# Kernel optimization log

Hardware: AMD Instinct MI355X
Metric: run time of the kernel (lower is better)

## Reference

```python
import jax, jax.numpy as jnp
import numpy as np

LEAK = 0.2
TEMP = 0.1          # CausalMask temperature
SPARSITY_W = 0.1
MI_W = 0.01
DAG_W = 1.0

def _leaky(x):
    return jax.nn.leaky_relu(x, LEAK)

def setup_inputs() -> dict:
    key = jax.random.key(0)
    B, F, S, H = 4096, 512, 32, 512
    H2, CH = H // 2, 64
    P = S * (S - 1) // 2  # 496 MI estimators
    ks = jax.random.split(key, 32)
    def w(k, shape, fan_in):
        return jax.random.normal(k, shape, jnp.float32) / np.sqrt(fan_in)
    return {
        'features': jax.random.normal(ks[0], (B, F), jnp.float32),
        'eps':      jax.random.normal(ks[1], (B, S), jnp.float32),
        'enc_w1': w(ks[2], (F, H), F),   'enc_b1': w(ks[3], (H,), H),
        'enc_w2': w(ks[4], (H, 2 * S), H), 'enc_b2': w(ks[5], (2 * S,), H) * 0.1,
        'log_weight': jax.random.normal(ks[6], (S, S), jnp.float32) * 0.5,
        'mech_w1': w(ks[7], (S, S, H2), S), 'mech_b1': w(ks[8], (S, H2), H2),
        'mech_w2': w(ks[9], (S, H2), H2),   'mech_b2': w(ks[10], (S,), H2),
        'dec_w1': w(ks[11], (S, H), S),  'dec_b1': w(ks[12], (H,), H),
        'dec_w2': w(ks[13], (H, F), H),  'dec_b2': w(ks[14], (F,), H),
        'mi_w1': w(ks[15], (P, 2, CH), 2),  'mi_b1': w(ks[16], (P, CH), CH),
        'mi_w2': w(ks[17], (P, CH, CH), CH), 'mi_b2': w(ks[18], (P, CH), CH),
        'mi_w3': w(ks[19], (P, CH), CH),     'mi_b3': w(ks[20], (P,), CH),
    }

def _forward(features, eps, enc_w1, enc_b1, enc_w2, enc_b2, log_weight,
             mech_w1, mech_b1, mech_w2, mech_b2, dec_w1, dec_b1, dec_w2, dec_b2,
             mi_w1, mi_b1, mi_w2, mi_b2, mi_w3, mi_b3):
    S = log_weight.shape[0]
    # ---- encode ----
    h = _leaky(features @ enc_w1 + enc_b1)
    params = h @ enc_w2 + enc_b2
    mean, log_std = jnp.split(params, 2, axis=-1)
    std = jnp.exp(log_std)
    z = mean + std * eps                                   # [B,S]
    # ---- soft causal adjacency (training mode) ----
    eye = jnp.eye(S, dtype=features.dtype)
    upper = jnp.triu(jnp.ones((S, S), features.dtype), k=1)
    lw = log_weight * upper - 10.0 * eye
    A = jax.nn.sigmoid(lw / TEMP)                          # [S,S]
    # ---- apply_causal_structure: stoch_dim tiny MLPs, vectorized ----
    # z_parents[b,i,s] = z[b,s] * A[s,i]
    zp = z[:, None, :] * A.T[None, :, :]                   # [B,S,S]
    h1 = _leaky(jnp.einsum('bis,ish->bih', zp, mech_w1) + mech_b1)  # [B,S,H2]
    z_causal = jnp.einsum('bih,ih->bi', h1, mech_w2) + mech_b2      # [B,S]
    # ---- decode ----
    recon = _leaky(z_causal @ dec_w1 + dec_b1) @ dec_w2 + dec_b2    # [B,F]
    # ---- losses ----
    recon_loss = jnp.mean((recon - features) ** 2)
    kl_loss = 0.5 * jnp.sum(mean ** 2 + std ** 2 - 2.0 * log_std - 1.0, axis=-1).mean()
    Asig = jax.nn.sigmoid(log_weight)
    sparsity_loss = jnp.sum(jnp.abs(Asig))
    # MI: one tiny MLP per (i<j) pair, row-major order == torch loop order
    iu, ju = jnp.triu_indices(S, k=1)
    pair = jnp.stack([z[:, iu], z[:, ju]], axis=-1)        # [B,P,2]
    m1 = _leaky(jnp.einsum('bpi,pih->bph', pair, mi_w1) + mi_b1)
    m2 = _leaky(jnp.einsum('bph,phk->bpk', m1, mi_w2) + mi_b2)
    mi_est = (jnp.einsum('bph,ph->bp', m2, mi_w3) + mi_b3).mean(0)  # [P]
    mi_loss = jnp.sum(jax.nn.sigmoid(log_weight[iu, ju]) * mi_est)
    # DAG: truncated matrix-exponential trace penalty
    A2 = Asig * Asig
    expm = eye
    mp = eye
    fact = 1.0
    for i in range(1, 10):
        fact *= i
        mp = mp @ A2
        expm = expm + mp / fact
    dag_loss = (jnp.trace(expm) - S) ** 2
    total_loss = recon_loss + kl_loss + SPARSITY_W * sparsity_loss + MI_W * mi_loss + DAG_W * dag_loss
    return z_causal, mean, std, recon, total_loss, recon_loss, kl_loss, sparsity_loss, mi_loss, dag_loss

def reference(features, eps, enc_w1, enc_b1, enc_w2, enc_b2, log_weight,
              mech_w1, mech_b1, mech_w2, mech_b2, dec_w1, dec_b1, dec_w2, dec_b2,
              mi_w1, mi_b1, mi_w2, mi_b2, mi_w3, mi_b3):
    return _forward(features, eps, enc_w1, enc_b1, enc_w2, enc_b2, log_weight,
                    mech_w1, mech_b1, mech_w2, mech_b2, dec_w1, dec_b1, dec_w2, dec_b2,
                    mi_w1, mi_b1, mi_w2, mi_b2, mi_w3, mi_b3)
```

## Files before the change

kernel.cpp:

```cpp
#include <hip/hip_runtime.h>
#include <hip/hip_bf16.h>

typedef float f32x4 __attribute__((ext_vector_type(4)));
typedef float f32x2 __attribute__((ext_vector_type(2)));
typedef short s16x8 __attribute__((ext_vector_type(8)));

__device__ __forceinline__ float leaky2(float x){ return fmaf(0.4f, fabsf(x), 0.6f * x); }

__device__ __forceinline__ short f2bf(float f){
    return __builtin_bit_cast(short, __float2bfloat16(f));
}

__global__ __launch_bounds__(256) void k_cvt(
    const float* __restrict__ feat, const float* __restrict__ ew1,
    const float* __restrict__ ew2, const float* __restrict__ dw2,
    const float* __restrict__ mw1, const float* __restrict__ mw2,
    const float* __restrict__ dw1,
    short* __restrict__ featbf, short* __restrict__ w1p,
    short* __restrict__ ew2p, short* __restrict__ dw2p,
    short* __restrict__ mw1p, short* __restrict__ mw2p,
    short* __restrict__ dw1p,
    const float* __restrict__ lw, float* __restrict__ A,
    float* __restrict__ acc)
{
    if (blockIdx.x >= 2048){
        __shared__ float A2s[1024], mp[1024], red[256];
        const int t = threadIdx.x;
        acc[t] = 0.f;
        acc[t + 256] = 0.f;
        float part = 0.f;
        #pragma unroll
        for (int q = 0; q < 4; ++q){
            int e = t * 4 + q;
            int r = e >> 5, c = e & 31;
            float v = lw[e];
            float sig = 1.f / (1.f + expf(-v));
            float l2 = (r < c) ? v * 10.f : ((r == c) ? -100.f : 0.f);
            A[e] = 1.f / (1.f + expf(-l2));
            part += sig;
            float a2 = sig * sig;
            A2s[e] = a2; mp[e] = a2;
        }
        red[t] = part; __syncthreads();
        for (int s = 128; s > 0; s >>= 1){ if (t < s) red[t] += red[t + s]; __syncthreads(); }
        if (t == 0) acc[2] = red[0];

        const float invf[10] = {0.f, 1.f, 0.5f, 1.6666667e-1f, 4.1666667e-2f,
                                8.3333333e-3f, 1.3888889e-3f, 1.9841270e-4f,
                                2.4801587e-5f, 2.7557319e-6f};
        float tr = 0.f;
        const int r = t >> 3, c0 = (t & 7) * 4;
        for (int n = 1; n <= 9; ++n){
            __syncthreads();
            if (t == 0){
                float s = 0.f;
                for (int k2 = 0; k2 < 32; ++k2) s += mp[k2 * 33];
                tr += s * invf[n];
            }
            if (n == 9) break;
            float av[4] = {0.f, 0.f, 0.f, 0.f};
            for (int k2 = 0; k2 < 32; ++k2){
                float m = mp[r * 32 + k2];
                #pragma unroll
                for (int q = 0; q < 4; ++q) av[q] = fmaf(m, A2s[k2 * 32 + c0 + q], av[q]);
            }
            __syncthreads();
            #pragma unroll
            for (int q = 0; q < 4; ++q) mp[r * 32 + c0 + q] = av[q];
        }
        if (t == 0) acc[3] = tr * tr;
        return;
    }
    for (int idx = blockIdx.x * 256 + threadIdx.x; idx < 620544; idx += 2048 * 256){
        int d = idx * 8;
        if (d < 2097152){
            f32x4 a0 = *(const f32x4*)&feat[d];
            f32x4 a1 = *(const f32x4*)&feat[d + 4];
            s16x8 v;
            #pragma unroll
            for (int e = 0; e < 4; ++e){ v[e] = f2bf(a0[e]); v[e + 4] = f2bf(a1[e]); }
            *(s16x8*)&featbf[d] = v;
            continue;
        }
        int s = d - 2097152;
        if (s < 262144){
            int t2 = s >> 9, lane = (s & 511) >> 3;
            int kb = (t2 & 15) * 32 + (lane >> 4) * 8;
            int n  = (t2 >> 4) * 16 + (lane & 15);
            s16x8 v;
            #pragma unroll
            for (int e = 0; e < 8; ++e) v[e] = f2bf(ew1[(kb + e) * 512 + n]);
            *(s16x8*)&w1p[s] = v;
            continue;
        }
        s -= 262144;
        if (s < 32768){
            int t2 = s >> 9, lane = (s & 511) >> 3;
            int kb = (t2 & 15) * 32 + (lane >> 4) * 8;
            int n  = (t2 >> 4) * 16 + (lane & 15);
            s16x8 v;
            #pragma unroll
            for (int e = 0; e < 8; ++e) v[e] = f2bf(ew2[(kb + e) * 64 + n]);
            *(s16x8*)&ew2p[s] = v;
            continue;
        }
        s -= 32768;
        if (s < 262144){
            int t2 = s >> 9, lane = (s & 511) >> 3;
            int kb = (t2 & 15) * 32 + (lane >> 4) * 8;
            int n  = (t2 >> 4) * 16 + (lane & 15);
            s16x8 v;
            #pragma unroll
            for (int e = 0; e < 8; ++e) v[e] = f2bf(dw2[(kb + e) * 512 + n]);
            *(s16x8*)&dw2p[s] = v;
            continue;
        }
        s -= 262144;
        if (s < 262144){
            int i = s >> 13, r2 = s & 8191;
            int nt = r2 >> 9, lane = (r2 & 511) >> 3;
            int kb = (lane >> 4) * 8;
            int n  = nt * 16 + (lane & 15);
            s16x8 v;
            #pragma unroll
            for (int e = 0; e < 8; ++e) v[e] = f2bf(mw1[i * 8192 + (kb + e) * 256 + n]);
            *(s16x8*)&mw1p[s] = v;
            continue;
        }
        s -= 262144;
        if (s < 2031616){
            int p = s >> 12, r2 = s & 4095;
            int tt = r2 >> 9, lane = (r2 & 511) >> 3;
            int nb = tt >> 1, ks = tt & 1;
            int kb = ks * 32 + (lane >> 4) * 8;
            int col = nb * 16 + (lane & 15);
            s16x8 v;
            #pragma unroll
            for (int e = 0; e < 8; ++e) v[e] = f2bf(mw2[(size_t)p * 4096 + (kb + e) * 64 + col]);
            *(s16x8*)&mw2p[s] = v;
            continue;
        }
        s -= 2031616;
        int nt = s >> 9, lane = (s & 511) >> 3;
        int kb = (lane >> 4) * 8;
        int n  = nt * 16 + (lane & 15);
        s16x8 v;
        #pragma unroll
        for (int e = 0; e < 8; ++e) v[e] = f2bf(dw1[(kb + e) * 512 + n]);
        *(s16x8*)&dw1p[s] = v;
    }
}

__global__ __launch_bounds__(512) void k_encf(
    const short* __restrict__ featbf, const short* __restrict__ w1p,
    const float* __restrict__ eb1, const short* __restrict__ ew2p,
    const float* __restrict__ eb2, const float* __restrict__ eps,
    float* __restrict__ omean, float* __restrict__ ostd,
    float* __restrict__ zt, float* __restrict__ accg)
{
    __shared__ short hlds[8192];
    __shared__ float P[16][65];
    __shared__ float zs[16][33];
    __shared__ float red[512];
    const int t = threadIdx.x, lane = t & 63, wv = t >> 6;
    const int ml = lane & 15, kg = lane >> 4;
    const int b0 = blockIdx.x * 16;

    f32x4 acc1[4] = {};
    for (int kt = 0; kt < 16; ++kt){
        s16x8 a = *(const s16x8*)&featbf[(size_t)(b0 + ml) * 512 + kt * 32 + kg * 8];
        #pragma unroll
        for (int nf = 0; nf < 4; ++nf){
            s16x8 b = *(const s16x8*)&w1p[((wv * 4 + nf) * 16 + kt) * 512 + lane * 8];
            acc1[nf] = __builtin_amdgcn_mfma_f32_16x16x32_bf16(a, b, acc1[nf], 0, 0, 0);
        }
    }
    #pragma unroll
    for (int nf = 0; nf < 4; ++nf){
        int col = wv * 64 + nf * 16 + ml;
        float bv = eb1[col];
        #pragma unroll
        for (int r = 0; r < 4; ++r){
            int row = kg * 4 + r;
            int byte = (row * 1024 + col * 2) ^ ((row & 7) << 4);
            hlds[byte >> 1] = f2bf(leaky2(acc1[nf][r] + bv));
        }
    }
    __syncthreads();

    if (wv < 4){
        f32x4 acc2 = {};
        for (int kt = 0; kt < 16; ++kt){
            int byte = (ml * 1024 + kt * 64 + kg * 16) ^ ((ml & 7) << 4);
            s16x8 a = *(const s16x8*)((const char*)hlds + byte);
            s16x8 b = *(const s16x8*)&ew2p[(wv * 16 + kt) * 512 + lane * 8];
            acc2 = __builtin_amdgcn_mfma_f32_16x16x32_bf16(a, b, acc2, 0, 0, 0);
        }
        int col = wv * 16 + ml;
        float bv = eb2[col];
        #pragma unroll
        for (int r = 0; r < 4; ++r)
            P[kg * 4 + r][col] = acc2[r] + bv;
    }
    __syncthreads();
    float klp = 0.f;
    {
        int row = t >> 5, n = t & 31;
        float mean = P[row][n], ls = P[row][n + 32];
        float sd = expf(ls);
        size_t o = (size_t)(b0 + row) * 32 + n;
        float z = fmaf(sd, eps[o], mean);
        omean[o] = mean; ostd[o] = sd;
        zs[row][n] = z;
        klp = mean * mean + sd * sd - 2.f * ls - 1.f;
    }
    __syncthreads();
    {
        int n = t >> 4, row = t & 15;
        zt[(size_t)n * 4096 + b0 + row] = zs[row][n];
    }
    red[t] = klp; __syncthreads();
    for (int s = 256; s > 0; s >>= 1){ if (t < s) red[t] += red[t + s]; __syncthreads(); }
    if (t == 0) atomicAdd(accg + 0, red[0]);
}

__global__ __launch_bounds__(256) void k_mimech(
    const float* __restrict__ zt,
    const float* __restrict__ w1g, const float* __restrict__ b1g,
    const short* __restrict__ w2p, const float* __restrict__ b2g,
    const float* __restrict__ w3g, float* __restrict__ macc,
    const float* __restrict__ A, const short* __restrict__ W1p,
    const float* __restrict__ mb1, const float* __restrict__ mw2,
    const float* __restrict__ mb2, float* __restrict__ out_zc)
{
    __shared__ float sA[32], sB1[256], sW2[256];
    const int t = threadIdx.x, lane = t & 63, wv = t >> 6;
    const int ml = lane & 15, kg = lane >> 4;
    if (blockIdx.x < 1984){
        const int p = blockIdx.x >> 2, bq = blockIdx.x & 3;
        int pi = 0, rem = p;
        while (rem >= 31 - pi){ rem -= 31 - pi; ++pi; }
        const int pj = pi + 1 + rem;

        const int zrow = wv * 16 + ml;
        const float* zi_b = zt + (size_t)pi * 4096 + bq * 1024 + zrow;
        const float* zj_b = zt + (size_t)pj * 4096 + bq * 1024 + zrow;

        f32x2 w10v[2][4], w11v[2][4], b1v[2][4];
        #pragma unroll
        for (int ks = 0; ks < 2; ++ks)
            #pragma unroll
            for (int q = 0; q < 4; ++q){
                int h = ks * 32 + kg * 8 + q * 2;
                w10v[ks][q] = *(const f32x2*)&w1g[p * 128 + h] * 0.6f;
                w11v[ks][q] = *(const f32x2*)&w1g[p * 128 + 64 + h] * 0.6f;
                b1v[ks][q]  = *(const f32x2*)&b1g[p * 64 + h] * 0.6f;
            }
        s16x8 bfr[4][2];
        f32x4 b2c[4];
        #pragma unroll
        for (int nb = 0; nb < 4; ++nb){
            float bv = b2g[p * 64 + nb * 16 + ml];
            b2c[nb][0] = bv; b2c[nb][1] = bv; b2c[nb][2] = bv; b2c[nb][3] = bv;
            #pragma unroll
            for (int ks = 0; ks < 2; ++ks)
                bfr[nb][ks] = *(const s16x8*)&w2p[(size_t)p * 4096 + (nb * 2 + ks) * 512 + lane * 8];
        }
        const f32x2 c23 = {0.66666669f, 0.66666669f};
        float slin[4] = {0.f, 0.f, 0.f, 0.f}, sabs[4] = {0.f, 0.f, 0.f, 0.f};
        #pragma unroll 1
        for (int tile = 0; tile < 16; ++tile){
            float zi_c = zi_b[tile * 64], zj_c = zj_b[tile * 64];
            f32x2 zi2 = {zi_c, zi_c}, zj2 = {zj_c, zj_c};
            s16x8 af0, af1;
            #pragma unroll
            for (int q = 0; q < 4; ++q){
                f32x2 m0 = __builtin_elementwise_fma(zi2, w10v[0][q],
                           __builtin_elementwise_fma(zj2, w11v[0][q], b1v[0][q]));
                m0 = __builtin_elementwise_fma(c23, __builtin_elementwise_abs(m0), m0);
                af0[q * 2] = f2bf(m0[0]); af0[q * 2 + 1] = f2bf(m0[1]);
                f32x2 m1 = __builtin_elementwise_fma(zi2, w10v[1][q],
                           __builtin_elementwise_fma(zj2, w11v[1][q], b1v[1][q]));
                m1 = __builtin_elementwise_fma(c23, __builtin_elementwise_abs(m1), m1);
                af1[q * 2] = f2bf(m1[0]); af1[q * 2 + 1] = f2bf(m1[1]);
            }
            #pragma unroll
            for (int nb = 0; nb < 4; ++nb){
                f32x4 d = __builtin_amdgcn_mfma_f32_16x16x32_bf16(af0, bfr[nb][0], b2c[nb], 0, 0, 0);
                d = __builtin_amdgcn_mfma_f32_16x16x32_bf16(af1, bfr[nb][1], d, 0, 0, 0);
                #pragma unroll
                for (int r2 = 0; r2 < 4; ++r2){
                    slin[nb] += d[r2];
                    sabs[nb] += fabsf(d[r2]);
                }
            }
        }
        float s = 0.f;
        #pragma unroll
        for (int nb = 0; nb < 4; ++nb){
            float w3 = w3g[p * 64 + nb * 16 + ml];
            s = fmaf(0.6f * w3, slin[nb], fmaf(0.4f * w3, sabs[nb], s));
        }
        #pragma unroll
        for (int off = 32; off; off >>= 1) s += __shfl_xor(s, off);
        if (lane == 0) atomicAdd(&macc[p], s);
    } else {
        const int bx = blockIdx.x - 1984;
        const int i = bx & 31;
        const int b0 = (bx >> 5) * 64 + wv * 16;
        if (t < 32) sA[t] = A[t * 32 + i];
        sB1[t] = mb1[i * 256 + t];
        sW2[t] = mw2[i * 256 + t];
        __syncthreads();
        float zv[8];
        #pragma unroll
        for (int q = 0; q < 8; ++q)
            zv[q] = zt[(size_t)(kg * 8 + q) * 4096 + b0 + ml];
        s16x8 af;
        #pragma unroll
        for (int q = 0; q < 8; ++q)
            af[q] = f2bf(zv[q] * sA[kg * 8 + q]);
        float s[4] = {0.f, 0.f, 0.f, 0.f};
        #pragma unroll
        for (int nt = 0; nt < 16; ++nt){
            s16x8 bf = *(const s16x8*)&W1p[i * 8192 + nt * 512 + lane * 8];
            int col = nt * 16 + ml;
            float b1e = sB1[col], w2v = sW2[col];
            f32x4 d;
            d[0] = b1e; d[1] = b1e; d[2] = b1e; d[3] = b1e;
            d = __builtin_amdgcn_mfma_f32_16x16x32_bf16(af, bf, d, 0, 0, 0);
            float w2a = 0.6f * w2v, w2b = 0.4f * w2v;
            #pragma unroll
            for (int r = 0; r < 4; ++r)
                s[r] = fmaf(w2a, d[r], fmaf(w2b, fabsf(d[r]), s[r]));
        }
        #pragma unroll
        for (int off = 1; off < 16; off <<= 1)
            #pragma unroll
            for (int r = 0; r < 4; ++r) s[r] += __shfl_xor(s[r], off);
        if (ml == 0){
            float bb = mb2[i];
            #pragma unroll
            for (int r = 0; r < 4; ++r){
                int b = b0 + kg * 4 + r;
                out_zc[(size_t)b * 32 + i] = s[r] + bb;
            }
        }
    }
}

__global__ __launch_bounds__(256) void k_decf(
    const float* __restrict__ zc, const short* __restrict__ dw1p,
    const float* __restrict__ db1, const short* __restrict__ dw2p,
    const float* __restrict__ db2, const float* __restrict__ feat,
    float* __restrict__ recon, float* __restrict__ accg)
{
    __shared__ short dlds[8192];
    __shared__ float red[256];
    const int t = threadIdx.x, lane = t & 63, wv = t >> 6;
    const int ml = lane & 15, kg = lane >> 4;
    const int b0 = blockIdx.x * 16;
    const int c0 = blockIdx.y * 128;

    s16x8 af;
    {
        int row = b0 + ml;
        f32x4 z0 = *(const f32x4*)&zc[(size_t)row * 32 + kg * 8];
        f32x4 z1 = *(const f32x4*)&zc[(size_t)row * 32 + kg * 8 + 4];
        #pragma unroll
        for (int e = 0; e < 4; ++e){
            af[e] = f2bf(z0[e]);
            af[e + 4] = f2bf(z1[e]);
        }
    }
    #pragma unroll
    for (int nf = 0; nf < 8; ++nf){
        int nt = wv * 8 + nf;
        s16x8 bf = *(const s16x8*)&dw1p[nt * 512 + lane * 8];
        int col = nt * 16 + ml;
        float b1e = db1[col];
        f32x4 c; c[0] = b1e; c[1] = b1e; c[2] = b1e; c[3] = b1e;
        f32x4 d = __builtin_amdgcn_mfma_f32_16x16x32_bf16(af, bf, c, 0, 0, 0);
        #pragma unroll
        for (int r = 0; r < 4; ++r){
            int row = kg * 4 + r;
            int byte = (row * 1024 + col * 2) ^ ((row & 7) << 4);
            dlds[byte >> 1] = f2bf(leaky2(d[r]));
        }
    }
    __syncthreads();

    f32x4 acc[2] = {};
    for (int kt = 0; kt < 16; ++kt){
        int byte = (ml * 1024 + kt * 64 + kg * 16) ^ ((ml & 7) << 4);
        s16x8 a = *(const s16x8*)((const char*)dlds + byte);
        #pragma unroll
        for (int j = 0; j < 2; ++j){
            int nt = (c0 >> 4) + wv * 2 + j;
            s16x8 b = *(const s16x8*)&dw2p[(nt * 16 + kt) * 512 + lane * 8];
            acc[j] = __builtin_amdgcn_mfma_f32_16x16x32_bf16(a, b, acc[j], 0, 0, 0);
        }
    }
    float lsum = 0.f;
    #pragma unroll
    for (int j = 0; j < 2; ++j){
        int col = c0 + (wv * 2 + j) * 16 + ml;
        float bv = db2[col];
        #pragma unroll
        for (int r = 0; r < 4; ++r){
            int row = b0 + kg * 4 + r;
            float v = acc[j][r] + bv;
            float d = v - feat[(size_t)row * 512 + col];
            lsum = fmaf(d, d, lsum);
            recon[(size_t)row * 512 + col] = v;
        }
    }
    red[t] = lsum; __syncthreads();
    for (int s = 128; s > 0; s >>= 1){ if (t < s) red[t] += red[t + s]; __syncthreads(); }
    if (t == 0) atomicAdd(accg + 1, red[0]);
}

__global__ void k_final(const float* __restrict__ acc, const float* __restrict__ lw,
                        const float* __restrict__ b3, float* __restrict__ outs)
{
    __shared__ float red[512];
    int t = threadIdx.x;
    float c = 0.f;
    if (t < 496){
        int pi = 0, rem = t;
        while (rem >= 31 - pi){ rem -= 31 - pi; ++pi; }
        int pj = pi + 1 + rem;
        float est = acc[4 + t] * (1.f / 4096.f) + b3[t];
        float w = 1.f / (1.f + expf(-lw[pi * 32 + pj]));
        c = w * est;
    }
    red[t] = c; __syncthreads();
    for (int s = 256; s > 0; s >>= 1){ if (t < s) red[t] += red[t + s]; __syncthreads(); }
    if (t == 0){
        float mi    = red[0];
        float recon = acc[1] * (1.f / (4096.f * 512.f));
        float kl    = 0.5f * acc[0] * (1.f / 4096.f);
        float sp    = acc[2], dag = acc[3];
        outs[0] = recon + kl + 0.1f * sp + 0.01f * mi + dag;
        outs[1] = recon; outs[2] = kl; outs[3] = sp; outs[4] = mi; outs[5] = dag;
    }
}

extern "C" void kernel_launch(void* const* d_in, const int* in_sizes, int n_in,
                              void* d_out, int out_size, void* d_ws, size_t ws_size,
                              hipStream_t stream)
{
    const float* features = (const float*)d_in[0];
    const float* eps      = (const float*)d_in[1];
    const float* enc_w1   = (const float*)d_in[2];
    const float* enc_b1   = (const float*)d_in[3];
    const float* enc_w2   = (const float*)d_in[4];
    const float* enc_b2   = (const float*)d_in[5];
    const float* log_w    = (const float*)d_in[6];
    const float* mech_w1  = (const float*)d_in[7];
    const float* mech_b1  = (const float*)d_in[8];
    const float* mech_w2  = (const float*)d_in[9];
    const float* mech_b2  = (const float*)d_in[10];
    const float* dec_w1   = (const float*)d_in[11];
    const float* dec_b1   = (const float*)d_in[12];
    const float* dec_w2   = (const float*)d_in[13];
    const float* dec_b2   = (const float*)d_in[14];
    const float* mi_w1    = (const float*)d_in[15];
    const float* mi_b1    = (const float*)d_in[16];
    const float* mi_w2    = (const float*)d_in[17];
    const float* mi_b2    = (const float*)d_in[18];
    const float* mi_w3    = (const float*)d_in[19];
    const float* mi_b3    = (const float*)d_in[20];

    float* W      = (float*)d_ws;
    float* zt     = W;
    float* Abuf   = W + 262144;
    float* accums = W + 263168;
    short* w1p    = (short*)(W + 263680);
    short* ew2p   = (short*)(W + 394752);
    short* dw2p   = (short*)(W + 411136);
    short* mw1p   = (short*)(W + 542208);
    short* mw2p   = (short*)(W + 673280);
    short* dw1p   = (short*)(W + 1689088);
    float* out    = (float*)d_out;
    short* featbf = (short*)(out + 393216);

    k_cvt<<<2049, 256, 0, stream>>>(features, enc_w1, enc_w2, dec_w2, mech_w1, mi_w2,
                                    dec_w1, featbf, w1p, ew2p, dw2p, mw1p, mw2p, dw1p,
                                    log_w, Abuf, accums);
    k_encf<<<256, 512, 0, stream>>>(featbf, w1p, enc_b1, ew2p, enc_b2, eps,
                                    out + 131072, out + 262144, zt, accums);
    k_mimech<<<4032, 256, 0, stream>>>(zt, mi_w1, mi_b1, mw2p, mi_b2, mi_w3, accums + 4,
                                       Abuf, mw1p, mech_b1, mech_w2, mech_b2, out);
    k_decf<<<dim3(256, 4), 256, 0, stream>>>(out, dw1p, dec_b1, dw2p, dec_b2, features,
                                             out + 393216, accums);
    k_final<<<1, 512, 0, stream>>>(accums, log_w, mi_b3, out + 2490368);
}
```

Measured before the change: 113.1 us.

## Move later-stage weight conversions into encoder kernel as extra blocks

```diff
diff --git a/kernel.cpp b/kernel.cpp
--- a/kernel.cpp
+++ b/kernel.cpp
@@ -13,13 +13,9 @@
 
 __global__ __launch_bounds__(256) void k_cvt(
     const float* __restrict__ feat, const float* __restrict__ ew1,
-    const float* __restrict__ ew2, const float* __restrict__ dw2,
-    const float* __restrict__ mw1, const float* __restrict__ mw2,
-    const float* __restrict__ dw1,
+    const float* __restrict__ ew2,
     short* __restrict__ featbf, short* __restrict__ w1p,
-    short* __restrict__ ew2p, short* __restrict__ dw2p,
-    short* __restrict__ mw1p, short* __restrict__ mw2p,
-    short* __restrict__ dw1p,
+    short* __restrict__ ew2p,
     const float* __restrict__ lw, float* __restrict__ A,
     float* __restrict__ acc)
 {
@@ -71,7 +67,7 @@
         if (t == 0) acc[3] = tr * tr;
         return;
     }
-    for (int idx = blockIdx.x * 256 + threadIdx.x; idx < 620544; idx += 2048 * 256){
+    for (int idx = blockIdx.x * 256 + threadIdx.x; idx < 299008; idx += 2048 * 256){
         int d = idx * 8;
         if (d < 2097152){
             f32x4 a0 = *(const f32x4*)&feat[d];
@@ -94,60 +90,13 @@
             continue;
         }
         s -= 262144;
-        if (s < 32768){
-            int t2 = s >> 9, lane = (s & 511) >> 3;
-            int kb = (t2 & 15) * 32 + (lane >> 4) * 8;
-            int n  = (t2 >> 4) * 16 + (lane & 15);
-            s16x8 v;
-            #pragma unroll
-            for (int e = 0; e < 8; ++e) v[e] = f2bf(ew2[(kb + e) * 64 + n]);
-            *(s16x8*)&ew2p[s] = v;
-            continue;
-        }
-        s -= 32768;
-        if (s < 262144){
-            int t2 = s >> 9, lane = (s & 511) >> 3;
-            int kb = (t2 & 15) * 32 + (lane >> 4) * 8;
-            int n  = (t2 >> 4) * 16 + (lane & 15);
-            s16x8 v;
-            #pragma unroll
-            for (int e = 0; e < 8; ++e) v[e] = f2bf(dw2[(kb + e) * 512 + n]);
-            *(s16x8*)&dw2p[s] = v;
-            continue;
-        }
-        s -= 262144;
-        if (s < 262144){
-            int i = s >> 13, r2 = s & 8191;
-            int nt = r2 >> 9, lane = (r2 & 511) >> 3;
-            int kb = (lane >> 4) * 8;
-            int n  = nt * 16 + (lane & 15);
-            s16x8 v;
-            #pragma unroll
-            for (int e = 0; e < 8; ++e) v[e] = f2bf(mw1[i * 8192 + (kb + e) * 256 + n]);
-            *(s16x8*)&mw1p[s] = v;
-            continue;
-        }
-        s -= 262144;
-        if (s < 2031616){
-            int p = s >> 12, r2 = s & 4095;
-            int tt = r2 >> 9, lane = (r2 & 511) >> 3;
-            int nb = tt >> 1, ks = tt & 1;
-            int kb = ks * 32 + (lane >> 4) * 8;
-            int col = nb * 16 + (lane & 15);
-            s16x8 v;
-            #pragma unroll
-            for (int e = 0; e < 8; ++e) v[e] = f2bf(mw2[(size_t)p * 4096 + (kb + e) * 64 + col]);
-            *(s16x8*)&mw2p[s] = v;
-            continue;
-        }
-        s -= 2031616;
-        int nt = s >> 9, lane = (s & 511) >> 3;
-        int kb = (lane >> 4) * 8;
-        int n  = nt * 16 + (lane & 15);
+        int t2 = s >> 9, lane = (s & 511) >> 3;
+        int kb = (t2 & 15) * 32 + (lane >> 4) * 8;
+        int n  = (t2 >> 4) * 16 + (lane & 15);
         s16x8 v;
         #pragma unroll
-        for (int e = 0; e < 8; ++e) v[e] = f2bf(dw1[(kb + e) * 512 + n]);
-        *(s16x8*)&dw1p[s] = v;
+        for (int e = 0; e < 8; ++e) v[e] = f2bf(ew2[(kb + e) * 64 + n]);
+        *(s16x8*)&ew2p[s] = v;
     }
 }
 
@@ -156,7 +105,11 @@
     const float* __restrict__ eb1, const short* __restrict__ ew2p,
     const float* __restrict__ eb2, const float* __restrict__ eps,
     float* __restrict__ omean, float* __restrict__ ostd,
-    float* __restrict__ zt, float* __restrict__ accg)
+    float* __restrict__ zt, float* __restrict__ accg,
+    const float* __restrict__ dw2, const float* __restrict__ mw1,
+    const float* __restrict__ mw2, const float* __restrict__ dw1,
+    short* __restrict__ dw2p, short* __restrict__ mw1p,
+    short* __restrict__ mw2p, short* __restrict__ dw1p)
 {
     __shared__ short hlds[8192];
     __shared__ float P[16][65];
@@ -164,6 +117,58 @@
     __shared__ float red[512];
     const int t = threadIdx.x, lane = t & 63, wv = t >> 6;
     const int ml = lane & 15, kg = lane >> 4;
+
+    if (blockIdx.x >= 256){
+        for (int idx = (blockIdx.x - 256) * 512 + t; idx < 321536; idx += 640 * 512){
+            int d = idx * 8;
+            if (d < 262144){
+                int s = d;
+                int t2 = s >> 9, lane2 = (s & 511) >> 3;
+                int kb = (t2 & 15) * 32 + (lane2 >> 4) * 8;
+                int n  = (t2 >> 4) * 16 + (lane2 & 15);
+                s16x8 v;
+                #pragma unroll
+                for (int e = 0; e < 8; ++e) v[e] = f2bf(dw2[(kb + e) * 512 + n]);
+                *(s16x8*)&dw2p[s] = v;
+                continue;
+            }
+            int s = d - 262144;
+            if (s < 262144){
+                int i = s >> 13, r2 = s & 8191;
+                int nt = r2 >> 9, lane2 = (r2 & 511) >> 3;
+                int kb = (lane2 >> 4) * 8;
+                int n  = nt * 16 + (lane2 & 15);
+                s16x8 v;
+                #pragma unroll
+                for (int e = 0; e < 8; ++e) v[e] = f2bf(mw1[i * 8192 + (kb + e) * 256 + n]);
+                *(s16x8*)&mw1p[s] = v;
+                continue;
+            }
+            s -= 262144;
+            if (s < 2031616){
+                int p = s >> 12, r2 = s & 4095;
+                int tt = r2 >> 9, lane2 = (r2 & 511) >> 3;
+                int nb = tt >> 1, ks = tt & 1;
+                int kb = ks * 32 + (lane2 >> 4) * 8;
+                int col = nb * 16 + (lane2 & 15);
+                s16x8 v;
+                #pragma unroll
+                for (int e = 0; e < 8; ++e) v[e] = f2bf(mw2[(size_t)p * 4096 + (kb + e) * 64 + col]);
+                *(s16x8*)&mw2p[s] = v;
+                continue;
+            }
+            s -= 2031616;
+            int nt = s >> 9, lane2 = (s & 511) >> 3;
+            int kb = (lane2 >> 4) * 8;
+            int n  = nt * 16 + (lane2 & 15);
+            s16x8 v;
+            #pragma unroll
+            for (int e = 0; e < 8; ++e) v[e] = f2bf(dw1[(kb + e) * 512 + n]);
+            *(s16x8*)&dw1p[s] = v;
+        }
+        return;
+    }
+
     const int b0 = blockIdx.x * 16;
 
     f32x4 acc1[4] = {};
@@ -485,11 +490,12 @@
     float* out    = (float*)d_out;
     short* featbf = (short*)(out + 393216);
 
-    k_cvt<<<2049, 256, 0, stream>>>(features, enc_w1, enc_w2, dec_w2, mech_w1, mi_w2,
-                                    dec_w1, featbf, w1p, ew2p, dw2p, mw1p, mw2p, dw1p,
-                                    log_w, Abuf, accums);
-    k_encf<<<256, 512, 0, stream>>>(featbf, w1p, enc_b1, ew2p, enc_b2, eps,
-                                    out + 131072, out + 262144, zt, accums);
+    k_cvt<<<2049, 256, 0, stream>>>(features, enc_w1, enc_w2,
+                                    featbf, w1p, ew2p, log_w, Abuf, accums);
+    k_encf<<<896, 512, 0, stream>>>(featbf, w1p, enc_b1, ew2p, enc_b2, eps,
+                                    out + 131072, out + 262144, zt, accums,
+                                    dec_w2, mech_w1, mi_w2, dec_w1,
+                                    dw2p, mw1p, mw2p, dw1p);
     k_mimech<<<4032, 256, 0, stream>>>(zt, mi_w1, mi_b1, mw2p, mi_b2, mi_w3, accums + 4,
                                        Abuf, mw1p, mech_b1, mech_w2, mech_b2, out);
     k_decf<<<dim3(256, 4), 256, 0, stream>>>(out, dw1p, dec_b1, dw2p, dec_b2, features,
```

After: 111.5 us (median of 2 runs). About the same (-1.4%).
